# Performance work log

Measured on AMD Instinct MI355X. Metric: run time of the kernel, lower is better.

Reference implementation:

```python
import jax, jax.numpy as jnp
import numpy as np

B, T, D = 8, 2048, 1024
E, S = 8, 1            # num_experts, num_slots
FF = 4 * (S * D)       # ffn_mult * (num_slots * hiddens)

def setup_inputs() -> dict:
    key = jax.random.key(0)
    ks = jax.random.split(key, 7)
    sd = S * D
    inp = {
        "X":  jax.random.normal(ks[0], (B, T, D), dtype=jnp.float32),
        # slots gating MLP (single linear D -> E*S)
        "Wg": jax.random.normal(ks[1], (D, E * S), dtype=jnp.float32) / np.sqrt(D),
        "bg": jnp.zeros((E * S,), dtype=jnp.float32),
        # expert FFN (weights SHARED across experts, as in source [FFN(...)]*E)
        "W1": jax.random.normal(ks[2], (sd, FF), dtype=jnp.float32) / np.sqrt(sd),
        "b1": jnp.zeros((FF,), dtype=jnp.float32),
        "W2": jax.random.normal(ks[3], (FF, sd), dtype=jnp.float32) / np.sqrt(FF),
        "b2": jnp.zeros((sd,), dtype=jnp.float32),
    }
    return inp

def reference(X, Wg, bg, W1, b1, W2, b2):
    # logits: (B, T, E*S)
    logits = jnp.einsum('btd,de->bte', X, Wg) + bg
    dispatch_w = jax.nn.softmax(logits, axis=1)   # over tokens T
    combine_w = jax.nn.softmax(logits, axis=2)    # over slots E*S
    # slots = dispatch_w^T @ X : (B, E*S, D) -> (B, E, S*D)
    slots = jnp.einsum('bte,btd->bed', dispatch_w, X).reshape(B, E, S * D)
    # shared-weight FFN applied per expert slot (dropout=0 at eval)
    h = jax.nn.silu(jnp.einsum('bef,fh->beh', slots, W1) + b1)
    y = jnp.einsum('beh,hf->bef', h, W2) + b2     # (B, E, S*D)
    y = y.reshape(B, E * S, D)
    # combine: (B, T, E*S) @ (B, E*S, D)
    return jnp.einsum('bte,bed->btd', combine_w, y)
```

## Files before the change

### kernel.cpp

```cpp
#include <hip/hip_runtime.h>
#include <math.h>

#define B_  8
#define T_  2048
#define D_  1024
#define E_  8
#define FF_ 4096
#define N_  64
#define BT_ (B_*T_)
#define WGS 1028

__global__ __launch_bounds__(256) void k_logits(
    const float* __restrict__ X, const float* __restrict__ Wg,
    const float* __restrict__ bg, float* __restrict__ logits,
    float* __restrict__ sumexp)
{
    __shared__ float wgT[E_ * WGS];

    const int tid  = threadIdx.x;
    const int lane = tid & 63;
    const int wv   = tid >> 6;

    #pragma unroll
    for (int r = 0; r < 32; ++r) {
        int idx = r * 256 + tid;
        wgT[(idx & 7) * WGS + (idx >> 3)] = Wg[idx];
    }
    __syncthreads();

    float4 w4[4][8];
    #pragma unroll
    for (int j = 0; j < 4; ++j)
        #pragma unroll
        for (int e = 0; e < 8; ++e)
            w4[j][e] = *(const float4*)&wgT[e * WGS + j * 256 + lane * 4];

    const int t0 = blockIdx.x * 64 + wv * 16;
    const int b  = t0 >> 11;
    const float bgv = bg[lane & 7];

    float se = 0.f;
    const float* xrow = &X[(size_t)t0 * D_ + lane * 4];

    float4 xc[4];
    #pragma unroll
    for (int j = 0; j < 4; ++j) xc[j] = *(const float4*)&xrow[j * 256];

    for (int t = 0; t < 16; ++t) {
        float4 xn[4];
        if (t < 15) {
            #pragma unroll
            for (int j = 0; j < 4; ++j)
                xn[j] = *(const float4*)&xrow[(size_t)(t + 1) * D_ + j * 256];
        }
        float acc[8];
        #pragma unroll
        for (int e = 0; e < 8; ++e) acc[e] = 0.f;
        #pragma unroll
        for (int j = 0; j < 4; ++j) {
            const float4 x = xc[j];
            #pragma unroll
            for (int e = 0; e < 8; ++e) {
                const float4 w = w4[j][e];
                acc[e] += x.x * w.x + x.y * w.y + x.z * w.z + x.w * w.w;
            }
        }
        #pragma unroll
        for (int j = 0; j < 4; ++j) xc[j] = xn[j];

        #pragma unroll
        for (int e = 0; e < 8; ++e) {
            acc[e] += __shfl_xor(acc[e], 1);
            acc[e] += __shfl_xor(acc[e], 2);
            acc[e] += __shfl_xor(acc[e], 4);
        }
        const float a01 = (lane & 1) ? acc[1] : acc[0];
        const float a23 = (lane & 1) ? acc[3] : acc[2];
        const float a45 = (lane & 1) ? acc[5] : acc[4];
        const float a67 = (lane & 1) ? acc[7] : acc[6];
        const float a03 = (lane & 2) ? a23 : a01;
        const float a47 = (lane & 2) ? a67 : a45;
        float v = (lane & 4) ? a47 : a03;
        v += __shfl_xor(v, 8);
        v += __shfl_xor(v, 16);
        v += __shfl_xor(v, 32);
        v += bgv;
        if (lane < 8) logits[(size_t)(t0 + t) * E_ + lane] = v;
        se += __expf(v);
    }
    if (lane < 8) atomicAdd(&sumexp[b * E_ + lane], se);
}

__global__ __launch_bounds__(256) void k_slots_part(
    const float* __restrict__ X, const float* __restrict__ logits,
    const float* __restrict__ sumexp, float* __restrict__ part)
{
    __shared__ float wlds[32 * 8];
    __shared__ float inv[8];

    const int tid = threadIdx.x;
    const int ts = blockIdx.x, b = blockIdx.y;
    const int t0 = ts * 32;

    if (tid < 8) inv[tid] = 1.f / sumexp[b * E_ + tid];
    __syncthreads();
    wlds[tid] = __expf(logits[(size_t)b * T_ * E_ + (size_t)t0 * E_ + tid]) * inv[tid & 7];
    __syncthreads();

    float4 acc[8];
    #pragma unroll
    for (int e = 0; e < 8; ++e) { acc[e].x = acc[e].y = acc[e].z = acc[e].w = 0.f; }

    const float* xb = &X[((size_t)b * T_ + t0) * D_ + tid * 4];
    #pragma unroll 8
    for (int t = 0; t < 32; ++t) {
        const float4 x4 = *(const float4*)&xb[(size_t)t * D_];
        const float4 wA = *(const float4*)&wlds[t * 8];
        const float4 wB = *(const float4*)&wlds[t * 8 + 4];
        const float w[8] = {wA.x, wA.y, wA.z, wA.w, wB.x, wB.y, wB.z, wB.w};
        #pragma unroll
        for (int e = 0; e < 8; ++e) {
            acc[e].x += x4.x * w[e];
            acc[e].y += x4.y * w[e];
            acc[e].z += x4.z * w[e];
            acc[e].w += x4.w * w[e];
        }
    }
    #pragma unroll
    for (int e = 0; e < 8; ++e) {
        *(float4*)&part[(size_t)ts * (N_ * D_) + (size_t)(b * E_ + e) * D_ + tid * 4] = acc[e];
    }
}

__global__ __launch_bounds__(256) void k_reduce_slots(
    const float* __restrict__ part, float* __restrict__ slots)
{
    const int i = blockIdx.x * 256 + threadIdx.x;
    float s = 0.f;
    #pragma unroll
    for (int p = 0; p < 64; ++p) s += part[(size_t)p * (N_ * D_) + i];
    slots[i] = s;
}

__global__ __launch_bounds__(256) void k_gemm_part(
    const float* __restrict__ A, const float* __restrict__ W,
    float* __restrict__ part, int K, int F)
{
    __shared__ float sT[32 * 68];

    const int tid = threadIdx.x;
    const int f0 = blockIdx.x * 512 + tid;
    const int k0 = blockIdx.y * 32;

    #pragma unroll
    for (int r = 0; r < 8; ++r) {
        int idx = r * 256 + tid;
        int n = idx >> 5, kk = idx & 31;
        sT[kk * 68 + n] = A[(size_t)n * K + k0 + kk];
    }
    __syncthreads();

    float acc0[64], acc1[64];
    #pragma unroll
    for (int n = 0; n < 64; ++n) { acc0[n] = 0.f; acc1[n] = 0.f; }

    #pragma unroll 8
    for (int kk = 0; kk < 32; ++kk) {
        const float w0 = W[(size_t)(k0 + kk) * F + f0];
        const float w1 = W[(size_t)(k0 + kk) * F + f0 + 256];
        const float4* sp = (const float4*)&sT[kk * 68];
        #pragma unroll
        for (int j = 0; j < 16; ++j) {
            const float4 s = sp[j];
            acc0[4*j+0] += s.x * w0; acc0[4*j+1] += s.y * w0;
            acc0[4*j+2] += s.z * w0; acc0[4*j+3] += s.w * w0;
            acc1[4*j+0] += s.x * w1; acc1[4*j+1] += s.y * w1;
            acc1[4*j+2] += s.z * w1; acc1[4*j+3] += s.w * w1;
        }
    }

    const size_t base = (size_t)blockIdx.y * N_ * F;
    #pragma unroll
    for (int n = 0; n < 64; ++n) {
        part[base + (size_t)n * F + f0]       = acc0[n];
        part[base + (size_t)n * F + f0 + 256] = acc1[n];
    }
}

__global__ __launch_bounds__(256) void k_reduce_silu(
    const float* __restrict__ part, const float* __restrict__ b1,
    float* __restrict__ h)
{
    const int i = blockIdx.x * 256 + threadIdx.x;
    float s = 0.f;
    #pragma unroll
    for (int p = 0; p < 32; ++p) s += part[(size_t)p * (N_ * FF_) + i];
    s += b1[i & (FF_ - 1)];
    h[i] = s / (1.f + __expf(-s));
}

__global__ __launch_bounds__(256) void k_reduce_bias(
    const float* __restrict__ part, const float* __restrict__ b2,
    float* __restrict__ y)
{
    const int i = blockIdx.x * 256 + threadIdx.x;
    float s = 0.f;
    #pragma unroll
    for (int p = 0; p < 128; ++p) s += part[(size_t)p * (N_ * D_) + i];
    y[i] = s + b2[i & (D_ - 1)];
}

__global__ __launch_bounds__(256) void k_combine(
    const float* __restrict__ logits, const float* __restrict__ y,
    float* __restrict__ out)
{
    __shared__ float wlds[64 * 8];
    const int tid = threadIdx.x;
    const int tc = blockIdx.x, b = blockIdx.y;
    const int t0 = tc * 64;

    if (tid < 64) {
        const float* lp = &logits[((size_t)b * T_ + t0 + tid) * E_];
        float ex[8]; float s = 0.f;
        #pragma unroll
        for (int i = 0; i < 8; ++i) { ex[i] = __expf(lp[i]); s += ex[i]; }
        const float invs = 1.f / s;
        #pragma unroll
        for (int i = 0; i < 8; ++i) wlds[tid * 8 + i] = ex[i] * invs;
    }
    __syncthreads();

    float4 yv[8];
    #pragma unroll
    for (int e = 0; e < 8; ++e)
        yv[e] = *(const float4*)&y[(size_t)(b * E_ + e) * D_ + tid * 4];

    #pragma unroll 4
    for (int t = 0; t < 64; ++t) {
        const float4 wA = *(const float4*)&wlds[t * 8];
        const float4 wB = *(const float4*)&wlds[t * 8 + 4];
        float4 a;
        a.x = wA.x*yv[0].x + wA.y*yv[1].x + wA.z*yv[2].x + wA.w*yv[3].x
            + wB.x*yv[4].x + wB.y*yv[5].x + wB.z*yv[6].x + wB.w*yv[7].x;
        a.y = wA.x*yv[0].y + wA.y*yv[1].y + wA.z*yv[2].y + wA.w*yv[3].y
            + wB.x*yv[4].y + wB.y*yv[5].y + wB.z*yv[6].y + wB.w*yv[7].y;
        a.z = wA.x*yv[0].z + wA.y*yv[1].z + wA.z*yv[2].z + wA.w*yv[3].z
            + wB.x*yv[4].z + wB.y*yv[5].z + wB.z*yv[6].z + wB.w*yv[7].z;
        a.w = wA.x*yv[0].w + wA.y*yv[1].w + wA.z*yv[2].w + wA.w*yv[3].w
            + wB.x*yv[4].w + wB.y*yv[5].w + wB.z*yv[6].w + wB.w*yv[7].w;
        *(float4*)&out[((size_t)b * T_ + t0 + t) * D_ + tid * 4] = a;
    }
}

extern "C" void kernel_launch(void* const* d_in, const int* in_sizes, int n_in,
                              void* d_out, int out_size, void* d_ws, size_t ws_size,
                              hipStream_t stream)
{
    const float* X  = (const float*)d_in[0];
    const float* Wg = (const float*)d_in[1];
    const float* bg = (const float*)d_in[2];
    const float* W1 = (const float*)d_in[3];
    const float* b1 = (const float*)d_in[4];
    const float* W2 = (const float*)d_in[5];
    const float* b2 = (const float*)d_in[6];
    float* out = (float*)d_out;

    float* wsf    = (float*)d_ws;
    float* logits = wsf;
    float* sumexp = logits + BT_ * E_;
    float* slots  = sumexp + 64;
    float* h      = slots + N_ * D_;
    float* y      = h + N_ * FF_;

    float* part = out;

    hipMemsetAsync(sumexp, 0, 64 * sizeof(float), stream);

    hipLaunchKernelGGL(k_logits,       dim3(BT_ / 64), dim3(256), 0, stream,
                       X, Wg, bg, logits, sumexp);
    hipLaunchKernelGGL(k_slots_part,   dim3(64, 8),    dim3(256), 0, stream,
                       X, logits, sumexp, part);
    hipLaunchKernelGGL(k_reduce_slots, dim3(256),      dim3(256), 0, stream,
                       part, slots);
    hipLaunchKernelGGL(k_gemm_part,    dim3(FF_ / 512, 1024 / 32), dim3(256), 0, stream,
                       slots, W1, part, 1024, FF_);
    hipLaunchKernelGGL(k_reduce_silu,  dim3(N_ * FF_ / 256), dim3(256), 0, stream,
                       part, b1, h);
    hipLaunchKernelGGL(k_gemm_part,    dim3(D_ / 512, FF_ / 32), dim3(256), 0, stream,
                       h, W2, part, FF_, D_);
    hipLaunchKernelGGL(k_reduce_bias,  dim3(N_ * D_ / 256), dim3(256), 0, stream,
                       part, b2, y);
    hipLaunchKernelGGL(k_combine,      dim3(32, 8), dim3(256), 0, stream,
                       logits, y, out);
}
```

Measured before the change: 285.9 us.

## Restructure slots reduction and FFN GEMMs, halve logits/combine tiles

Replaces the partial-sum slots kernel and its reduction with a precomputed dispatch-weight buffer and a single k_slots kernel that reduces over all tokens in-block using shuffles and LDS. This removes a large partial buffer round trip. The FFN GEMMs become a templated kernel that keeps W in registers and reads A rows as broadcast float4, with larger K splits, so the reduce kernels sum fewer partials. k_logits and k_combine now use 32-token blocks, doubling their block counts. The cost is an extra dispatch kernel and buffer, and a k_slots grid of only 256 blocks, each walking all 2048 tokens.

```diff
diff --git a/kernel.cpp b/kernel.cpp
--- a/kernel.cpp
+++ b/kernel.cpp
@@ -35,7 +35,7 @@
         for (int e = 0; e < 8; ++e)
             w4[j][e] = *(const float4*)&wgT[e * WGS + j * 256 + lane * 4];
 
-    const int t0 = blockIdx.x * 64 + wv * 16;
+    const int t0 = blockIdx.x * 32 + wv * 8;
     const int b  = t0 >> 11;
     const float bgv = bg[lane & 7];
 
@@ -46,9 +46,9 @@
     #pragma unroll
     for (int j = 0; j < 4; ++j) xc[j] = *(const float4*)&xrow[j * 256];
 
-    for (int t = 0; t < 16; ++t) {
+    for (int t = 0; t < 8; ++t) {
         float4 xn[4];
-        if (t < 15) {
+        if (t < 7) {
             #pragma unroll
             for (int j = 0; j < 4; ++j)
                 xn[j] = *(const float4*)&xrow[(size_t)(t + 1) * D_ + j * 256];
@@ -91,100 +91,128 @@
     if (lane < 8) atomicAdd(&sumexp[b * E_ + lane], se);
 }
 
-__global__ __launch_bounds__(256) void k_slots_part(
-    const float* __restrict__ X, const float* __restrict__ logits,
-    const float* __restrict__ sumexp, float* __restrict__ part)
-{
-    __shared__ float wlds[32 * 8];
-    __shared__ float inv[8];
-
+__global__ __launch_bounds__(256) void k_dispatch(
+    const float* __restrict__ logits, const float* __restrict__ sumexp,
+    float* __restrict__ dw)
+{
+    const int idx = blockIdx.x * 256 + threadIdx.x;
+    const int e = idx & 7, b = idx >> 14;
+    dw[idx] = __expf(logits[idx]) / sumexp[b * E_ + e];
+}
+
+__global__ __launch_bounds__(256) void k_slots(
+    const float* __restrict__ X, const float* __restrict__ dw,
+    float* __restrict__ slots)
+{
+    __shared__ float dwl[E_ * 516];
+    __shared__ float4 red4[4 * 64];
+
+    const int tid  = threadIdx.x;
+    const int lane = tid & 63;
+    const int wv   = tid >> 6;
+    const int t_sub = lane >> 3;
+    const int d4    = lane & 7;
+    const int d0 = blockIdx.x * 32;
+    const int b  = blockIdx.y;
+
+    float4 acc[8];
+    #pragma unroll
+    for (int e = 0; e < 8; ++e) { acc[e].x = acc[e].y = acc[e].z = acc[e].w = 0.f; }
+
+    const float* xp = &X[((size_t)b * T_ + wv * 8 + t_sub) * D_ + d0 + d4 * 4];
+    const float* dwg = &dw[(size_t)b * T_ * E_];
+
+    for (int p = 0; p < 4; ++p) {
+        __syncthreads();
+        #pragma unroll
+        for (int r = 0; r < 4; ++r) {
+            const int i4 = r * 256 + tid;
+            const float4 v = *(const float4*)&dwg[(size_t)p * 4096 + i4 * 4];
+            const int t = i4 >> 1, e0 = (i4 & 1) * 4;
+            dwl[(e0 + 0) * 516 + t] = v.x;
+            dwl[(e0 + 1) * 516 + t] = v.y;
+            dwl[(e0 + 2) * 516 + t] = v.z;
+            dwl[(e0 + 3) * 516 + t] = v.w;
+        }
+        __syncthreads();
+
+        #pragma unroll 8
+        for (int it = 0; it < 16; ++it) {
+            const int tl = wv * 8 + t_sub + it * 32;
+            const float4 x = *(const float4*)&xp[((size_t)p * 512 + it * 32) * D_];
+            #pragma unroll
+            for (int e = 0; e < 8; ++e) {
+                const float w = dwl[e * 516 + tl];
+                acc[e].x += w * x.x; acc[e].y += w * x.y;
+                acc[e].z += w * x.z; acc[e].w += w * x.w;
+            }
+        }
+    }
+
+    #pragma unroll
+    for (int e = 0; e < 8; ++e) {
+        #pragma unroll
+        for (int m = 8; m <= 32; m <<= 1) {
+            acc[e].x += __shfl_xor(acc[e].x, m);
+            acc[e].y += __shfl_xor(acc[e].y, m);
+            acc[e].z += __shfl_xor(acc[e].z, m);
+            acc[e].w += __shfl_xor(acc[e].w, m);
+        }
+    }
+    if (t_sub == 0) {
+        #pragma unroll
+        for (int e = 0; e < 8; ++e) red4[wv * 64 + e * 8 + d4] = acc[e];
+    }
+    __syncthreads();
+    if (tid < 64) {
+        const int e = tid >> 3, dd = tid & 7;
+        float4 s = red4[e * 8 + dd];
+        #pragma unroll
+        for (int w = 1; w < 4; ++w) {
+            const float4 r = red4[w * 64 + e * 8 + dd];
+            s.x += r.x; s.y += r.y; s.z += r.z; s.w += r.w;
+        }
+        *(float4*)&slots[(size_t)(b * E_ + e) * D_ + d0 + dd * 4] = s;
+    }
+}
+
+template<int KTOT, int FTOT, int KR, int FB, int NSPL>
+__global__ __launch_bounds__(256) void k_gemm(
+    const float* __restrict__ A, const float* __restrict__ W,
+    float* __restrict__ part)
+{
     const int tid = threadIdx.x;
-    const int ts = blockIdx.x, b = blockIdx.y;
-    const int t0 = ts * 32;
-
-    if (tid < 8) inv[tid] = 1.f / sumexp[b * E_ + tid];
-    __syncthreads();
-    wlds[tid] = __expf(logits[(size_t)b * T_ * E_ + (size_t)t0 * E_ + tid]) * inv[tid & 7];
-    __syncthreads();
-
-    float4 acc[8];
-    #pragma unroll
-    for (int e = 0; e < 8; ++e) { acc[e].x = acc[e].y = acc[e].z = acc[e].w = 0.f; }
-
-    const float* xb = &X[((size_t)b * T_ + t0) * D_ + tid * 4];
-    #pragma unroll 8
-    for (int t = 0; t < 32; ++t) {
-        const float4 x4 = *(const float4*)&xb[(size_t)t * D_];
-        const float4 wA = *(const float4*)&wlds[t * 8];
-        const float4 wB = *(const float4*)&wlds[t * 8 + 4];
-        const float w[8] = {wA.x, wA.y, wA.z, wA.w, wB.x, wB.y, wB.z, wB.w};
-        #pragma unroll
-        for (int e = 0; e < 8; ++e) {
-            acc[e].x += x4.x * w[e];
-            acc[e].y += x4.y * w[e];
-            acc[e].z += x4.z * w[e];
-            acc[e].w += x4.w * w[e];
-        }
-    }
-    #pragma unroll
-    for (int e = 0; e < 8; ++e) {
-        *(float4*)&part[(size_t)ts * (N_ * D_) + (size_t)(b * E_ + e) * D_ + tid * 4] = acc[e];
-    }
-}
-
-__global__ __launch_bounds__(256) void k_reduce_slots(
-    const float* __restrict__ part, float* __restrict__ slots)
-{
-    const int i = blockIdx.x * 256 + threadIdx.x;
-    float s = 0.f;
-    #pragma unroll
-    for (int p = 0; p < 64; ++p) s += part[(size_t)p * (N_ * D_) + i];
-    slots[i] = s;
-}
-
-__global__ __launch_bounds__(256) void k_gemm_part(
-    const float* __restrict__ A, const float* __restrict__ W,
-    float* __restrict__ part, int K, int F)
-{
-    __shared__ float sT[32 * 68];
-
-    const int tid = threadIdx.x;
-    const int f0 = blockIdx.x * 512 + tid;
-    const int k0 = blockIdx.y * 32;
-
-    #pragma unroll
-    for (int r = 0; r < 8; ++r) {
-        int idx = r * 256 + tid;
-        int n = idx >> 5, kk = idx & 31;
-        sT[kk * 68 + n] = A[(size_t)n * K + k0 + kk];
-    }
-    __syncthreads();
-
-    float acc0[64], acc1[64];
-    #pragma unroll
-    for (int n = 0; n < 64; ++n) { acc0[n] = 0.f; acc1[n] = 0.f; }
-
-    #pragma unroll 8
-    for (int kk = 0; kk < 32; ++kk) {
-        const float w0 = W[(size_t)(k0 + kk) * F + f0];
-        const float w1 = W[(size_t)(k0 + kk) * F + f0 + 256];
-        const float4* sp = (const float4*)&sT[kk * 68];
-        #pragma unroll
-        for (int j = 0; j < 16; ++j) {
-            const float4 s = sp[j];
-            acc0[4*j+0] += s.x * w0; acc0[4*j+1] += s.y * w0;
-            acc0[4*j+2] += s.z * w0; acc0[4*j+3] += s.w * w0;
-            acc1[4*j+0] += s.x * w1; acc1[4*j+1] += s.y * w1;
-            acc1[4*j+2] += s.z * w1; acc1[4*j+3] += s.w * w1;
-        }
-    }
-
-    const size_t base = (size_t)blockIdx.y * N_ * F;
-    #pragma unroll
-    for (int n = 0; n < 64; ++n) {
-        part[base + (size_t)n * F + f0]       = acc0[n];
-        part[base + (size_t)n * F + f0 + 256] = acc1[n];
-    }
+    const int fi = tid % FB;
+    const int f  = blockIdx.x * FB + fi;
+    const int k0 = blockIdx.y * KR;
+    constexpr int NR = 64 / NSPL;
+    const int nbase = __builtin_amdgcn_readfirstlane((tid / FB) * NR);
+
+    float w[KR];
+    #pragma unroll
+    for (int kk = 0; kk < KR; ++kk)
+        w[kk] = W[(size_t)(k0 + kk) * FTOT + f];
+
+    float acc[NR];
+    #pragma unroll
+    for (int j = 0; j < NR; ++j) acc[j] = 0.f;
+
+    #pragma unroll 4
+    for (int j = 0; j < NR; ++j) {
+        const float* ar = &A[(size_t)(nbase + j) * KTOT + k0];
+        float a = 0.f; (void)a;
+        #pragma unroll
+        for (int k4 = 0; k4 < KR / 4; ++k4) {
+            const float4 av = *(const float4*)&ar[k4 * 4];
+            acc[j] += av.x * w[k4*4+0] + av.y * w[k4*4+1]
+                    + av.z * w[k4*4+2] + av.w * w[k4*4+3];
+        }
+    }
+
+    const size_t base = (size_t)blockIdx.y * N_ * FTOT;
+    #pragma unroll
+    for (int j = 0; j < NR; ++j)
+        part[base + (size_t)(nbase + j) * FTOT + f] = acc[j];
 }
 
 __global__ __launch_bounds__(256) void k_reduce_silu(
@@ -194,7 +222,7 @@
     const int i = blockIdx.x * 256 + threadIdx.x;
     float s = 0.f;
     #pragma unroll
-    for (int p = 0; p < 32; ++p) s += part[(size_t)p * (N_ * FF_) + i];
+    for (int p = 0; p < 16; ++p) s += part[(size_t)p * (N_ * FF_) + i];
     s += b1[i & (FF_ - 1)];
     h[i] = s / (1.f + __expf(-s));
 }
@@ -206,7 +234,7 @@
     const int i = blockIdx.x * 256 + threadIdx.x;
     float s = 0.f;
     #pragma unroll
-    for (int p = 0; p < 128; ++p) s += part[(size_t)p * (N_ * D_) + i];
+    for (int p = 0; p < 32; ++p) s += part[(size_t)p * (N_ * D_) + i];
     y[i] = s + b2[i & (D_ - 1)];
 }
 
@@ -214,12 +242,12 @@
     const float* __restrict__ logits, const float* __restrict__ y,
     float* __restrict__ out)
 {
-    __shared__ float wlds[64 * 8];
+    __shared__ float wlds[32 * 8];
     const int tid = threadIdx.x;
     const int tc = blockIdx.x, b = blockIdx.y;
-    const int t0 = tc * 64;
-
-    if (tid < 64) {
+    const int t0 = tc * 32;
+
+    if (tid < 32) {
         const float* lp = &logits[((size_t)b * T_ + t0 + tid) * E_];
         float ex[8]; float s = 0.f;
         #pragma unroll
@@ -236,7 +264,7 @@
         yv[e] = *(const float4*)&y[(size_t)(b * E_ + e) * D_ + tid * 4];
 
     #pragma unroll 4
-    for (int t = 0; t < 64; ++t) {
+    for (int t = 0; t < 32; ++t) {
         const float4 wA = *(const float4*)&wlds[t * 8];
         const float4 wB = *(const float4*)&wlds[t * 8 + 4];
         float4 a;
@@ -271,25 +299,28 @@
     float* slots  = sumexp + 64;
     float* h      = slots + N_ * D_;
     float* y      = h + N_ * FF_;
+    float* dwbuf  = y + N_ * D_;
 
     float* part = out;
 
     hipMemsetAsync(sumexp, 0, 64 * sizeof(float), stream);
 
-    hipLaunchKernelGGL(k_logits,       dim3(BT_ / 64), dim3(256), 0, stream,
+    hipLaunchKernelGGL(k_logits,   dim3(BT_ / 32), dim3(256), 0, stream,
                        X, Wg, bg, logits, sumexp);
-    hipLaunchKernelGGL(k_slots_part,   dim3(64, 8),    dim3(256), 0, stream,
-                       X, logits, sumexp, part);
-    hipLaunchKernelGGL(k_reduce_slots, dim3(256),      dim3(256), 0, stream,
-                       part, slots);
-    hipLaunchKernelGGL(k_gemm_part,    dim3(FF_ / 512, 1024 / 32), dim3(256), 0, stream,
-                       slots, W1, part, 1024, FF_);
-    hipLaunchKernelGGL(k_reduce_silu,  dim3(N_ * FF_ / 256), dim3(256), 0, stream,
+    hipLaunchKernelGGL(k_dispatch, dim3(BT_ * E_ / 256), dim3(256), 0, stream,
+                       logits, sumexp, dwbuf);
+    hipLaunchKernelGGL(k_slots,    dim3(32, 8), dim3(256), 0, stream,
+                       X, dwbuf, slots);
+    hipLaunchKernelGGL(HIP_KERNEL_NAME(k_gemm<1024, 4096, 64, 256, 1>),
+                       dim3(4096 / 256, 1024 / 64), dim3(256), 0, stream,
+                       slots, W1, part);
+    hipLaunchKernelGGL(k_reduce_silu, dim3(N_ * FF_ / 256), dim3(256), 0, stream,
                        part, b1, h);
-    hipLaunchKernelGGL(k_gemm_part,    dim3(D_ / 512, FF_ / 32), dim3(256), 0, stream,
-                       h, W2, part, FF_, D_);
-    hipLaunchKernelGGL(k_reduce_bias,  dim3(N_ * D_ / 256), dim3(256), 0, stream,
+    hipLaunchKernelGGL(HIP_KERNEL_NAME(k_gemm<4096, 1024, 128, 128, 2>),
+                       dim3(1024 / 128, 4096 / 128), dim3(256), 0, stream,
+                       h, W2, part);
+    hipLaunchKernelGGL(k_reduce_bias, dim3(N_ * D_ / 256), dim3(256), 0, stream,
                        part, b2, y);
-    hipLaunchKernelGGL(k_combine,      dim3(32, 8), dim3(256), 0, stream,
+    hipLaunchKernelGGL(k_combine,  dim3(64, 8), dim3(256), 0, stream,
                        logits, y, out);
 }
```

Measured after the change: 362.2 us. +26.7%, slower.
